# Kernel optimization log

Measured on AMD Instinct MI355X. Metric: run time of the kernel, lower is better.

The kernel has to match this reference:

```python
import jax, jax.numpy as jnp
import numpy as np

B, S, D_MODEL = 2, 2048, 1024
N_HEADS, N_KV_HEADS, D_HEAD = 16, 4, 64
N_GROUPS = N_HEADS // N_KV_HEADS
ATTN_SCALE = 1.0 / np.sqrt(D_HEAD)  # qk_scale_factor=1.0
LOGIT_SOFTCAP = 15.0
WINDOW = 256
N_GLOBAL = 4
EPS = 1e-8


def _l2_normalize(x):
    norm = jnp.linalg.norm(x, axis=-1, keepdims=True)
    return x / (norm + EPS)


def _apply_rope(t, cos, sin):
    # t: (B, H, S, D); cos/sin: (S, D//2)
    half = t.shape[-1] // 2
    x1, x2 = t[..., :half], t[..., half:]
    c = cos[None, None, :, :]
    s = sin[None, None, :, :]
    return jnp.concatenate([x1 * c - x2 * s, x1 * s + x2 * c], axis=-1)


def _sliding_window_mask(seq_len, window, n_global):
    q = jnp.arange(seq_len)[:, None]
    k = jnp.arange(seq_len)[None, :]
    causal = k <= q
    in_window = k > q - window
    is_global = k < n_global
    return (causal & in_window | is_global)[None, None, :, :]


def setup_inputs() -> dict:
    key = jax.random.key(0)
    ks = jax.random.split(key, 7)
    x = jax.random.normal(ks[0], (B, S, D_MODEL), dtype=jnp.float32)
    # RoPE tables from standard inverse-frequency construction
    inv_freq = 1.0 / (10000.0 ** (jnp.arange(0, D_HEAD, 2, dtype=jnp.float32) / D_HEAD))
    angles = jnp.arange(S, dtype=jnp.float32)[:, None] * inv_freq[None, :]  # (S, D_HEAD//2)
    cos = jnp.cos(angles)
    sin = jnp.sin(angles)
    # causal mask supplied by caller (TransformerLM): (1,1,S,S) bool, True = attend
    mask = (jnp.arange(S)[None, :] <= jnp.arange(S)[:, None])[None, None, :, :]
    scale_in = 1.0 / np.sqrt(D_MODEL)
    Wq = jax.random.normal(ks[1], (D_MODEL, N_HEADS * D_HEAD), dtype=jnp.float32) * scale_in
    Wk = jax.random.normal(ks[2], (D_MODEL, N_KV_HEADS * D_HEAD), dtype=jnp.float32) * scale_in
    Wv = jax.random.normal(ks[3], (D_MODEL, N_KV_HEADS * D_HEAD), dtype=jnp.float32) * scale_in
    Wo = jax.random.normal(ks[4], (N_HEADS * D_HEAD, D_MODEL), dtype=jnp.float32) * (1.0 / np.sqrt(N_HEADS * D_HEAD))
    return {"x": x, "cos": cos, "sin": sin, "mask": mask, "Wq": Wq, "Wk": Wk, "Wv": Wv, "Wo": Wo}


def reference(x, cos, sin, mask, Wq, Wk, Wv, Wo):
    Bb, Ss, _ = x.shape
    q = (x @ Wq).reshape(Bb, Ss, N_HEADS, D_HEAD).transpose(0, 2, 1, 3)      # (B,H,S,D)
    k = (x @ Wk).reshape(Bb, Ss, N_KV_HEADS, D_HEAD).transpose(0, 2, 1, 3)   # (B,Hkv,S,D)
    v = (x @ Wv).reshape(Bb, Ss, N_KV_HEADS, D_HEAD).transpose(0, 2, 1, 3)
    # QK L2 normalization (in fp32)
    q = _l2_normalize(q.astype(jnp.float32)).astype(q.dtype)
    k = _l2_normalize(k.astype(jnp.float32)).astype(k.dtype)
    # RoPE
    q = _apply_rope(q, cos, sin)
    k = _apply_rope(k, cos, sin)
    # GQA: expand kv heads
    k_exp = jnp.repeat(k, N_GROUPS, axis=1)
    v_exp = jnp.repeat(v, N_GROUPS, axis=1)
    scores = jnp.einsum('bhqd,bhkd->bhqk', q.astype(jnp.float32), k_exp.astype(jnp.float32)) * ATTN_SCALE
    scores = LOGIT_SOFTCAP * jnp.tanh(scores / LOGIT_SOFTCAP)
    window_mask = _sliding_window_mask(Ss, WINDOW, N_GLOBAL)
    combined = mask & window_mask
    scores = jnp.where(combined, scores, jnp.float32(-1e9))
    weights = jax.nn.softmax(scores, axis=-1)
    context = jnp.einsum('bhqk,bhkd->bhqd', weights, v_exp.astype(jnp.float32))
    context = context.transpose(0, 2, 1, 3).reshape(Bb, Ss, N_HEADS * D_HEAD).astype(x.dtype)
    return context @ Wo
```

## Files before the change

### kernel.cpp

```cpp
#include <hip/hip_runtime.h>
#include <hip/hip_bf16.h>

#define BATCH 2
#define SLEN 2048
#define DMODEL 1024
#define NHEADS 16
#define NKV 4
#define DHEAD 64
#define WINDOW 256
#define NGLOBAL 4

typedef __attribute__((ext_vector_type(8))) short short8;
typedef __attribute__((ext_vector_type(4))) float floatx4;

__device__ __forceinline__ ushort f2bf(float f) {
    __hip_bfloat16 h = __float2bfloat16(f);
    return *reinterpret_cast<ushort*>(&h);
}
__device__ __forceinline__ float bf2f(ushort u) {
    __hip_bfloat16 h = *reinterpret_cast<__hip_bfloat16*>(&u);
    return __bfloat162float(h);
}
__device__ __forceinline__ bool is_bf16_inputs(const uint* cosu) {
    return (cosu[0] & 0xFFFFu) != 0u;
}
__device__ __forceinline__ void gload_lds16(const ushort* g, ushort* l) {
    __builtin_amdgcn_global_load_lds(
        (const __attribute__((address_space(1))) void*)g,
        (__attribute__((address_space(3))) void*)l, 16, 0, 0);
}

__global__ __launch_bounds__(256) void prep_all(const void* __restrict__ x,
                                                const void* __restrict__ cosi,
                                                const void* __restrict__ sini,
                                                const void* __restrict__ Wq,
                                                const void* __restrict__ Wk,
                                                const void* __restrict__ Wv,
                                                const void* __restrict__ Wo,
                                                ushort* __restrict__ xb,
                                                float* __restrict__ cosf,
                                                float* __restrict__ sinf,
                                                ushort* __restrict__ Wt,
                                                ushort* __restrict__ Wot,
                                                const uint* __restrict__ cosu)
{
    __shared__ ushort t[32][33];
    const bool isbf = is_bf16_inputs(cosu);
    const int bid = blockIdx.x, tid = threadIdx.x;
    if (bid < 2048) {
        size_t i = (size_t)bid * 256 + tid;
        size_t e = i * 8;
        if (isbf) {
            *reinterpret_cast<uint4*>(xb + e) = reinterpret_cast<const uint4*>(x)[i];
        } else {
            const float* f = reinterpret_cast<const float*>(x) + e;
            ushort o[8];
#pragma unroll
            for (int j = 0; j < 8; ++j) o[j] = f2bf(f[j]);
            *reinterpret_cast<uint4*>(xb + e) = *reinterpret_cast<uint4*>(o);
        }
        return;
    }
    if (bid < 2560) {
        int i = (bid - 2048) * 256 + tid;
        const void* src = (i < SLEN * 32) ? cosi : sini;
        float* dst = (i < SLEN * 32) ? cosf : sinf;
        int e = i & (SLEN * 32 - 1);
        dst[e] = isbf ? bf2f(reinterpret_cast<const ushort*>(src)[e])
                      : reinterpret_cast<const float*>(src)[e];
        return;
    }
    const void* src; ushort* dst; int C, tl;
    if (bid < 3584)      { src = Wq; dst = Wt;                       C = 1024; tl = bid - 2560; }
    else if (bid < 3840) { src = Wk; dst = Wt + (size_t)1024 * 1024; C = 256;  tl = bid - 3584; }
    else if (bid < 4096) { src = Wv; dst = Wt + (size_t)1280 * 1024; C = 256;  tl = bid - 3840; }
    else                 { src = Wo; dst = Wot;                      C = 1024; tl = bid - 4096; }
    const int nbx = C >> 5;
    const int bx = (tl % nbx) * 32, by = (tl / nbx) * 32;
    const int tx = tid & 31, ty = tid >> 5;
#pragma unroll
    for (int j = 0; j < 32; j += 8) {
        size_t idx = (size_t)(by + ty + j) * C + bx + tx;
        t[ty + j][tx] = isbf ? reinterpret_cast<const ushort*>(src)[idx]
                             : f2bf(reinterpret_cast<const float*>(src)[idx]);
    }
    __syncthreads();
#pragma unroll
    for (int j = 0; j < 32; j += 8)
        dst[(size_t)(bx + ty + j) * 1024 + by + tx] = t[tx][ty + j];
}

__global__ __launch_bounds__(256) void gemm_qkv_nr(const ushort* __restrict__ A,
                                                   const ushort* __restrict__ Bt,
                                                   const float* __restrict__ cosf,
                                                   const float* __restrict__ sinf,
                                                   ushort* __restrict__ Qb,
                                                   ushort* __restrict__ Kg,
                                                   ushort* __restrict__ Vtg)
{
    __shared__ __align__(16) ushort buf[12288];
    ushort* lsA = buf;
    ushort* lsB = buf + 8192;
    const int tid = threadIdx.x;
    const int lane = tid & 63, w = tid >> 6;
    const int ln15 = lane & 15, quad = lane >> 4;
    const int z = blockIdx.x;
    const int rm = blockIdx.y * 128;
    const int cn = z * 64;

    floatx4 acc[2][4];
#pragma unroll
    for (int i = 0; i < 2; ++i)
#pragma unroll
        for (int j = 0; j < 4; ++j) acc[i][j] = (floatx4){0.f, 0.f, 0.f, 0.f};

    for (int k0 = 0; k0 < 1024; k0 += 64) {
        __syncthreads();
#pragma unroll
        for (int i = 0; i < 4; ++i) {
            const int c = (i * 4 + w) * 64 + lane;
            const int row = c >> 3, col = (c & 7) * 8;
            gload_lds16(&A[(size_t)(rm + row) * 1024 + k0 + col], &lsA[(i * 4 + w) * 512]);
        }
#pragma unroll
        for (int i = 0; i < 2; ++i) {
            const int c = (w * 2 + i) * 64 + lane;
            const int row = c >> 3, col = (c & 7) * 8;
            gload_lds16(&Bt[(size_t)(cn + row) * 1024 + k0 + col], &lsB[(w * 2 + i) * 512]);
        }
        __syncthreads();
#pragma unroll
        for (int kk = 0; kk < 64; kk += 32) {
            short8 af[2], bv[4];
#pragma unroll
            for (int i = 0; i < 2; ++i)
                af[i] = *reinterpret_cast<const short8*>(&lsA[(w * 32 + i * 16 + ln15) * 64 + kk + quad * 8]);
#pragma unroll
            for (int j = 0; j < 4; ++j)
                bv[j] = *reinterpret_cast<const short8*>(&lsB[(j * 16 + ln15) * 64 + kk + quad * 8]);
#pragma unroll
            for (int i = 0; i < 2; ++i)
#pragma unroll
                for (int j = 0; j < 4; ++j)
                    acc[i][j] = __builtin_amdgcn_mfma_f32_16x16x32_bf16(af[i], bv[j], acc[i][j], 0, 0, 0);
        }
    }

    __syncthreads();
    const int b = rm >> 11, s0 = rm & (SLEN - 1);

    if (z < 20) {
#pragma unroll
        for (int i = 0; i < 2; ++i) {
#pragma unroll
            for (int r = 0; r < 4; ++r) {
                const int row_l = w * 32 + i * 16 + quad * 4 + r;
                float v0 = acc[i][0][r], v1 = acc[i][1][r], v2 = acc[i][2][r], v3 = acc[i][3][r];
                float ss = v0 * v0 + v1 * v1 + v2 * v2 + v3 * v3;
                ss += __shfl_xor(ss, 1, 64);
                ss += __shfl_xor(ss, 2, 64);
                ss += __shfl_xor(ss, 4, 64);
                ss += __shfl_xor(ss, 8, 64);
                const float inv = 1.f / (sqrtf(ss) + 1e-8f);
                const float n0 = v0 * inv, n1 = v1 * inv, n2 = v2 * inv, n3 = v3 * inv;
                const int spos = s0 + row_l;
                const float c0 = cosf[spos * 32 + ln15],      c1 = cosf[spos * 32 + 16 + ln15];
                const float sn0 = sinf[spos * 32 + ln15],     sn1 = sinf[spos * 32 + 16 + ln15];
                buf[row_l * 72 + ln15]      = f2bf(n0 * c0 - n2 * sn0);
                buf[row_l * 72 + 16 + ln15] = f2bf(n1 * c1 - n3 * sn1);
                buf[row_l * 72 + 32 + ln15] = f2bf(n0 * sn0 + n2 * c0);
                buf[row_l * 72 + 48 + ln15] = f2bf(n1 * sn1 + n3 * c1);
            }
        }
        __syncthreads();
        ushort* dst = (z < 16) ? Qb + ((size_t)(b * NHEADS + z) * SLEN + s0) * 64
                               : Kg + ((size_t)(b * NKV + (z - 16)) * SLEN + s0) * 64;
#pragma unroll
        for (int it = 0; it < 4; ++it) {
            const int c = it * 256 + tid;
            const int row = c >> 3, col = (c & 7) * 8;
            *reinterpret_cast<uint4*>(dst + (size_t)row * 64 + col) =
                *reinterpret_cast<const uint4*>(&buf[row * 72 + col]);
        }
    } else {
#pragma unroll
        for (int i = 0; i < 2; ++i)
#pragma unroll
            for (int r = 0; r < 4; ++r) {
                const int row_l = w * 32 + i * 16 + quad * 4 + r;
#pragma unroll
                for (int j = 0; j < 4; ++j)
                    buf[(j * 16 + ln15) * 136 + row_l] = f2bf(acc[i][j][r]);
            }
        __syncthreads();
        ushort* dst = Vtg + ((size_t)(b * NKV + (z - 20)) * 64) * SLEN;
#pragma unroll
        for (int it = 0; it < 4; ++it) {
            const int c = it * 256 + tid;
            const int d = c >> 4, sb = (c & 15) * 8;
            *reinterpret_cast<uint4*>(dst + (size_t)d * SLEN + s0 + sb) =
                *reinterpret_cast<const uint4*>(&buf[d * 136 + sb]);
        }
    }
}

__global__ __launch_bounds__(256) void attn_mfma(const ushort* __restrict__ Qb,
                                                 const ushort* __restrict__ Kg,
                                                 const ushort* __restrict__ Vtg,
                                                 ushort* __restrict__ ctx)
{
    __shared__ ushort Ks[64 * 72];
    __shared__ ushort Vs[64 * 72];
    __shared__ ushort Ps[4][16 * 72];

    const int tid = threadIdx.x;
    const int lane = tid & 63, w = tid >> 6;
    const int ln15 = lane & 15, quad = lane >> 4;
    const int bid = blockIdx.x;
    const int qt = bid & 31, bh = bid >> 5;
    const int h = bh & (NHEADS - 1), b = bh >> 4, hkv = h >> 2;
    const int q0 = qt * 64;
    const int qw = q0 + w * 16;

    const ushort* Qrow = Qb + ((size_t)bh * SLEN + qw) * 64;
    const ushort* Kbase = Kg + (size_t)(b * NKV + hkv) * SLEN * 64;
    const ushort* Vbase = Vtg + (size_t)(b * NKV + hkv) * 64 * SLEN;

    short8 qf0 = *reinterpret_cast<const short8*>(Qrow + (size_t)ln15 * 64 + quad * 8);
    short8 qf1 = *reinterpret_cast<const short8*>(Qrow + (size_t)ln15 * 64 + 32 + quad * 8);

    floatx4 O0 = {0,0,0,0}, O1 = {0,0,0,0}, O2 = {0,0,0,0}, O3 = {0,0,0,0};
    float lp[4] = {0.f, 0.f, 0.f, 0.f};

    int kminA = q0 - (WINDOW - 1); if (kminA < 0) kminA = 0;
    kminA &= ~63;
    const int gmax = kminA < NGLOBAL ? kminA : NGLOBAL;
    const int nc = (q0 + 64 - kminA) >> 6;

    for (int c = (gmax > 0 ? -1 : 0); c < nc; ++c) {
        const int kbase = (c < 0) ? 0 : kminA + c * 64;
        __syncthreads();
#pragma unroll
        for (int j = 0; j < 2; ++j) {
            const int c2 = tid + j * 256;
            const int row = c2 >> 3, col = (c2 & 7) * 8;
            *reinterpret_cast<uint4*>(&Ks[row * 72 + col]) =
                *reinterpret_cast<const uint4*>(&Kbase[(size_t)(kbase + row) * 64 + col]);
            *reinterpret_cast<uint4*>(&Vs[row * 72 + col]) =
                *reinterpret_cast<const uint4*>(&Vbase[(size_t)row * SLEN + kbase + col]);
        }
        __syncthreads();

#pragma unroll
        for (int t = 0; t < 4; ++t) {
            short8 kf0 = *reinterpret_cast<const short8*>(&Ks[(t * 16 + ln15) * 72 + quad * 8]);
            short8 kf1 = *reinterpret_cast<const short8*>(&Ks[(t * 16 + ln15) * 72 + 32 + quad * 8]);
            floatx4 sc = {0,0,0,0};
            sc = __builtin_amdgcn_mfma_f32_16x16x32_bf16(qf0, kf0, sc, 0, 0, 0);
            sc = __builtin_amdgcn_mfma_f32_16x16x32_bf16(qf1, kf1, sc, 0, 0, 0);
            const int k = kbase + t * 16 + ln15;
#pragma unroll
            for (int r = 0; r < 4; ++r) {
                const int q = qw + quad * 4 + r;
                const bool valid = (c < 0) ? (k < gmax)
                                           : (k <= q && (k + WINDOW > q || k < NGLOBAL));
                float sv = sc[r] * 0.125f;
                float e2 = __expf(sv * 0.13333333f);
                float st = 15.f - 30.f * __builtin_amdgcn_rcpf(e2 + 1.f);
                ushort eb = valid ? f2bf(__expf(st)) : (ushort)0;
                Ps[w][(quad * 4 + r) * 72 + t * 16 + ln15] = eb;
                lp[r] += bf2f(eb);
            }
        }
        short8 af0 = *reinterpret_cast<const short8*>(&Ps[w][ln15 * 72 + quad * 8]);
        short8 af1 = *reinterpret_cast<const short8*>(&Ps[w][ln15 * 72 + 32 + quad * 8]);
#pragma unroll
        for (int n = 0; n < 4; ++n) {
            short8 vf0 = *reinterpret_cast<const short8*>(&Vs[(n * 16 + ln15) * 72 + quad * 8]);
            short8 vf1 = *reinterpret_cast<const short8*>(&Vs[(n * 16 + ln15) * 72 + 32 + quad * 8]);
            floatx4 On = (n == 0) ? O0 : (n == 1) ? O1 : (n == 2) ? O2 : O3;
            On = __builtin_amdgcn_mfma_f32_16x16x32_bf16(af0, vf0, On, 0, 0, 0);
            On = __builtin_amdgcn_mfma_f32_16x16x32_bf16(af1, vf1, On, 0, 0, 0);
            if (n == 0) O0 = On; else if (n == 1) O1 = On; else if (n == 2) O2 = On; else O3 = On;
        }
    }

#pragma unroll
    for (int r = 0; r < 4; ++r) {
#pragma unroll
        for (int off = 1; off < 16; off <<= 1)
            lp[r] += __shfl_xor(lp[r], off, 64);
        const float inv = __builtin_amdgcn_rcpf(lp[r]);
        const int q = qw + quad * 4 + r;
        ushort* crow = ctx + ((size_t)(b * SLEN + q)) * DMODEL + h * 64 + ln15;
        crow[0]  = f2bf(O0[r] * inv);
        crow[16] = f2bf(O1[r] * inv);
        crow[32] = f2bf(O2[r] * inv);
        crow[48] = f2bf(O3[r] * inv);
    }
}

__global__ __launch_bounds__(256) void gemm_out(const ushort* __restrict__ A,
                                                const ushort* __restrict__ Bt,
                                                void* __restrict__ out,
                                                const uint* __restrict__ cosu)
{
    __shared__ __align__(16) ushort buf[12288];
    ushort* lsA = buf;
    ushort* lsB = buf + 8192;
    const int tid = threadIdx.x;
    const int lane = tid & 63, w = tid >> 6;
    const int ln15 = lane & 15, quad = lane >> 4;
    const int rm = blockIdx.y * 128;
    const int cn = blockIdx.x * 64;

    floatx4 acc[2][4];
#pragma unroll
    for (int i = 0; i < 2; ++i)
#pragma unroll
        for (int j = 0; j < 4; ++j) acc[i][j] = (floatx4){0.f, 0.f, 0.f, 0.f};

    for (int k0 = 0; k0 < 1024; k0 += 64) {
        __syncthreads();
#pragma unroll
        for (int i = 0; i < 4; ++i) {
            const int c = (i * 4 + w) * 64 + lane;
            const int row = c >> 3, col = (c & 7) * 8;
            gload_lds16(&A[(size_t)(rm + row) * 1024 + k0 + col], &lsA[(i * 4 + w) * 512]);
        }
#pragma unroll
        for (int i = 0; i < 2; ++i) {
            const int c = (w * 2 + i) * 64 + lane;
            const int row = c >> 3, col = (c & 7) * 8;
            gload_lds16(&Bt[(size_t)(cn + row) * 1024 + k0 + col], &lsB[(w * 2 + i) * 512]);
        }
        __syncthreads();
#pragma unroll
        for (int kk = 0; kk < 64; kk += 32) {
            short8 af[2], bv[4];
#pragma unroll
            for (int i = 0; i < 2; ++i)
                af[i] = *reinterpret_cast<const short8*>(&lsA[(w * 32 + i * 16 + ln15) * 64 + kk + quad * 8]);
#pragma unroll
            for (int j = 0; j < 4; ++j)
                bv[j] = *reinterpret_cast<const short8*>(&lsB[(j * 16 + ln15) * 64 + kk + quad * 8]);
#pragma unroll
            for (int i = 0; i < 2; ++i)
#pragma unroll
                for (int j = 0; j < 4; ++j)
                    acc[i][j] = __builtin_amdgcn_mfma_f32_16x16x32_bf16(af[i], bv[j], acc[i][j], 0, 0, 0);
        }
    }

    const bool outbf = is_bf16_inputs(cosu);
#pragma unroll
    for (int i = 0; i < 2; ++i) {
#pragma unroll
        for (int r = 0; r < 4; ++r) {
            const int grow = rm + w * 32 + i * 16 + quad * 4 + r;
#pragma unroll
            for (int j = 0; j < 4; ++j) {
                const int gcol = cn + j * 16 + ln15;
                if (outbf) reinterpret_cast<ushort*>(out)[(size_t)grow * DMODEL + gcol] = f2bf(acc[i][j][r]);
                else       reinterpret_cast<float*>(out)[(size_t)grow * DMODEL + gcol] = acc[i][j][r];
            }
        }
    }
}

extern "C" void kernel_launch(void* const* d_in, const int* in_sizes, int n_in,
                              void* d_out, int out_size, void* d_ws, size_t ws_size,
                              hipStream_t stream)
{
    (void)in_sizes; (void)n_in; (void)out_size; (void)ws_size;
    const void* x = d_in[0];
    const void* cosi = d_in[1];
    const void* sini = d_in[2];
    const uint* cosu = (const uint*)d_in[1];
    const void* Wq = d_in[4];
    const void* Wk = d_in[5];
    const void* Wv = d_in[6];
    const void* Wo = d_in[7];

    ushort* xb = (ushort*)d_ws;
    ushort* Wt = xb + (size_t)4096 * 1024;
    ushort* Wot = Wt + (size_t)1536 * 1024;
    float* cosf = (float*)(Wot + (size_t)1024 * 1024);
    float* sinf = cosf + (size_t)SLEN * 32;
    ushort* Qbf = (ushort*)(sinf + (size_t)SLEN * 32);
    ushort* Kgf = Qbf + (size_t)BATCH * NHEADS * SLEN * 64;
    ushort* Vtg = Kgf + (size_t)BATCH * NKV * SLEN * 64;
    ushort* ctx = Vtg + (size_t)BATCH * NKV * 64 * SLEN;

    prep_all<<<dim3(5120), 256, 0, stream>>>(x, cosi, sini, Wq, Wk, Wv, Wo,
                                             xb, cosf, sinf, Wt, Wot, cosu);

    gemm_qkv_nr<<<dim3(24, 32), 256, 0, stream>>>(xb, Wt, cosf, sinf, Qbf, Kgf, Vtg);

    attn_mfma<<<dim3(BATCH * NHEADS * SLEN / 64), 256, 0, stream>>>(Qbf, Kgf, Vtg, ctx);

    gemm_out<<<dim3(16, 32), 256, 0, stream>>>(ctx, Wot, d_out, cosu);
}
```

Measured before the change: 166.1 us.

## Fuse prep, QKV GEMM, attention and output GEMM into one cooperative persistent kernel

Replaces the four separate kernel launches with a single cooperative megakernel that loops over virtual blocks per stage and separates stages with grid-wide syncs. This is meant to remove launch gaps and tail effects between stages. The output GEMM is retiled to 64x64 tiles to give more tiles. Softcap tanh is replaced by a cubic Taylor approximation, and row sums now use unrounded fp32 probabilities. The change risks grid.sync overhead, lower occupancy under the fused register budget, and accuracy loss from the tanh approximation.

```diff
diff --git a/kernel.cpp b/kernel.cpp
--- a/kernel.cpp
+++ b/kernel.cpp
@@ -1,5 +1,8 @@
 #include <hip/hip_runtime.h>
 #include <hip/hip_bf16.h>
+#include <hip/hip_cooperative_groups.h>
+
+namespace cg = cooperative_groups;
 
 #define BATCH 2
 #define SLEN 2048
@@ -30,340 +33,305 @@
         (__attribute__((address_space(3))) void*)l, 16, 0, 0);
 }
 
-__global__ __launch_bounds__(256) void prep_all(const void* __restrict__ x,
-                                                const void* __restrict__ cosi,
-                                                const void* __restrict__ sini,
-                                                const void* __restrict__ Wq,
-                                                const void* __restrict__ Wk,
-                                                const void* __restrict__ Wv,
-                                                const void* __restrict__ Wo,
-                                                ushort* __restrict__ xb,
-                                                float* __restrict__ cosf,
-                                                float* __restrict__ sinf,
-                                                ushort* __restrict__ Wt,
-                                                ushort* __restrict__ Wot,
-                                                const uint* __restrict__ cosu)
+__global__ __launch_bounds__(256, 4) void mega(
+    const void* __restrict__ x, const void* __restrict__ cosi, const void* __restrict__ sini,
+    const void* __restrict__ Wq, const void* __restrict__ Wk,
+    const void* __restrict__ Wv, const void* __restrict__ Wo,
+    ushort* __restrict__ xb, float* __restrict__ cosf_, float* __restrict__ sinf_,
+    ushort* __restrict__ Wt, ushort* __restrict__ Wot,
+    ushort* __restrict__ Qb, ushort* __restrict__ Kg, ushort* __restrict__ Vtg,
+    ushort* __restrict__ ctx, void* __restrict__ out,
+    const uint* __restrict__ cosu, int nblk)
 {
-    __shared__ ushort t[32][33];
-    const bool isbf = is_bf16_inputs(cosu);
-    const int bid = blockIdx.x, tid = threadIdx.x;
-    if (bid < 2048) {
-        size_t i = (size_t)bid * 256 + tid;
-        size_t e = i * 8;
-        if (isbf) {
-            *reinterpret_cast<uint4*>(xb + e) = reinterpret_cast<const uint4*>(x)[i];
-        } else {
-            const float* f = reinterpret_cast<const float*>(x) + e;
-            ushort o[8];
-#pragma unroll
-            for (int j = 0; j < 8; ++j) o[j] = f2bf(f[j]);
-            *reinterpret_cast<uint4*>(xb + e) = *reinterpret_cast<uint4*>(o);
-        }
-        return;
-    }
-    if (bid < 2560) {
-        int i = (bid - 2048) * 256 + tid;
-        const void* src = (i < SLEN * 32) ? cosi : sini;
-        float* dst = (i < SLEN * 32) ? cosf : sinf;
-        int e = i & (SLEN * 32 - 1);
-        dst[e] = isbf ? bf2f(reinterpret_cast<const ushort*>(src)[e])
-                      : reinterpret_cast<const float*>(src)[e];
-        return;
-    }
-    const void* src; ushort* dst; int C, tl;
-    if (bid < 3584)      { src = Wq; dst = Wt;                       C = 1024; tl = bid - 2560; }
-    else if (bid < 3840) { src = Wk; dst = Wt + (size_t)1024 * 1024; C = 256;  tl = bid - 3584; }
-    else if (bid < 4096) { src = Wv; dst = Wt + (size_t)1280 * 1024; C = 256;  tl = bid - 3840; }
-    else                 { src = Wo; dst = Wot;                      C = 1024; tl = bid - 4096; }
-    const int nbx = C >> 5;
-    const int bx = (tl % nbx) * 32, by = (tl / nbx) * 32;
-    const int tx = tid & 31, ty = tid >> 5;
-#pragma unroll
-    for (int j = 0; j < 32; j += 8) {
-        size_t idx = (size_t)(by + ty + j) * C + bx + tx;
-        t[ty + j][tx] = isbf ? reinterpret_cast<const ushort*>(src)[idx]
-                             : f2bf(reinterpret_cast<const float*>(src)[idx]);
-    }
-    __syncthreads();
-#pragma unroll
-    for (int j = 0; j < 32; j += 8)
-        dst[(size_t)(bx + ty + j) * 1024 + by + tx] = t[tx][ty + j];
-}
-
-__global__ __launch_bounds__(256) void gemm_qkv_nr(const ushort* __restrict__ A,
-                                                   const ushort* __restrict__ Bt,
-                                                   const float* __restrict__ cosf,
-                                                   const float* __restrict__ sinf,
-                                                   ushort* __restrict__ Qb,
-                                                   ushort* __restrict__ Kg,
-                                                   ushort* __restrict__ Vtg)
-{
-    __shared__ __align__(16) ushort buf[12288];
-    ushort* lsA = buf;
-    ushort* lsB = buf + 8192;
+    __shared__ __align__(16) ushort sm[13824];
+    cg::grid_group grid = cg::this_grid();
     const int tid = threadIdx.x;
+    const int blk = blockIdx.x;
     const int lane = tid & 63, w = tid >> 6;
     const int ln15 = lane & 15, quad = lane >> 4;
-    const int z = blockIdx.x;
-    const int rm = blockIdx.y * 128;
-    const int cn = z * 64;
-
-    floatx4 acc[2][4];
-#pragma unroll
-    for (int i = 0; i < 2; ++i)
-#pragma unroll
-        for (int j = 0; j < 4; ++j) acc[i][j] = (floatx4){0.f, 0.f, 0.f, 0.f};
-
-    for (int k0 = 0; k0 < 1024; k0 += 64) {
-        __syncthreads();
-#pragma unroll
-        for (int i = 0; i < 4; ++i) {
-            const int c = (i * 4 + w) * 64 + lane;
-            const int row = c >> 3, col = (c & 7) * 8;
-            gload_lds16(&A[(size_t)(rm + row) * 1024 + k0 + col], &lsA[(i * 4 + w) * 512]);
-        }
-#pragma unroll
-        for (int i = 0; i < 2; ++i) {
-            const int c = (w * 2 + i) * 64 + lane;
-            const int row = c >> 3, col = (c & 7) * 8;
-            gload_lds16(&Bt[(size_t)(cn + row) * 1024 + k0 + col], &lsB[(w * 2 + i) * 512]);
+    const bool isbf = is_bf16_inputs(cosu);
+
+    for (int vb = blk; vb < 5120; vb += nblk) {
+        if (vb < 2048) {
+            size_t i = (size_t)vb * 256 + tid;
+            size_t e = i * 8;
+            if (isbf) {
+                *reinterpret_cast<uint4*>(xb + e) = reinterpret_cast<const uint4*>(x)[i];
+            } else {
+                const float* f = reinterpret_cast<const float*>(x) + e;
+                ushort o[8];
+#pragma unroll
+                for (int j = 0; j < 8; ++j) o[j] = f2bf(f[j]);
+                *reinterpret_cast<uint4*>(xb + e) = *reinterpret_cast<uint4*>(o);
+            }
+        } else if (vb < 2560) {
+            int i = (vb - 2048) * 256 + tid;
+            const void* src = (i < SLEN * 32) ? cosi : sini;
+            float* dst = (i < SLEN * 32) ? cosf_ : sinf_;
+            int e = i & (SLEN * 32 - 1);
+            dst[e] = isbf ? bf2f(reinterpret_cast<const ushort*>(src)[e])
+                          : reinterpret_cast<const float*>(src)[e];
+        } else {
+            const void* src; ushort* dst; int C, tl;
+            if (vb < 3584)      { src = Wq; dst = Wt;                       C = 1024; tl = vb - 2560; }
+            else if (vb < 3840) { src = Wk; dst = Wt + (size_t)1024 * 1024; C = 256;  tl = vb - 3584; }
+            else if (vb < 4096) { src = Wv; dst = Wt + (size_t)1280 * 1024; C = 256;  tl = vb - 3840; }
+            else                { src = Wo; dst = Wot;                      C = 1024; tl = vb - 4096; }
+            const int nbx = C >> 5;
+            const int bx = (tl % nbx) * 32, by = (tl / nbx) * 32;
+            const int tx = tid & 31, ty = tid >> 5;
+            ushort (*t)[33] = reinterpret_cast<ushort(*)[33]>(sm);
+#pragma unroll
+            for (int j = 0; j < 32; j += 8) {
+                size_t idx = (size_t)(by + ty + j) * C + bx + tx;
+                t[ty + j][tx] = isbf ? reinterpret_cast<const ushort*>(src)[idx]
+                                     : f2bf(reinterpret_cast<const float*>(src)[idx]);
+            }
+            __syncthreads();
+#pragma unroll
+            for (int j = 0; j < 32; j += 8)
+                dst[(size_t)(bx + ty + j) * 1024 + by + tx] = t[tx][ty + j];
         }
         __syncthreads();
-#pragma unroll
-        for (int kk = 0; kk < 64; kk += 32) {
-            short8 af[2], bv[4];
+    }
+    grid.sync();
+
+    {
+        ushort* lsA = sm;
+        ushort* lsB = sm + 8192;
+        for (int tile = blk; tile < 768; tile += nblk) {
+            const int z = tile % 24;
+            const int rm = (tile / 24) * 128;
+            const int cn = z * 64;
+
+            floatx4 acc[2][4];
 #pragma unroll
             for (int i = 0; i < 2; ++i)
-                af[i] = *reinterpret_cast<const short8*>(&lsA[(w * 32 + i * 16 + ln15) * 64 + kk + quad * 8]);
-#pragma unroll
-            for (int j = 0; j < 4; ++j)
-                bv[j] = *reinterpret_cast<const short8*>(&lsB[(j * 16 + ln15) * 64 + kk + quad * 8]);
-#pragma unroll
-            for (int i = 0; i < 2; ++i)
-#pragma unroll
-                for (int j = 0; j < 4; ++j)
-                    acc[i][j] = __builtin_amdgcn_mfma_f32_16x16x32_bf16(af[i], bv[j], acc[i][j], 0, 0, 0);
+#pragma unroll
+                for (int j = 0; j < 4; ++j) acc[i][j] = (floatx4){0.f, 0.f, 0.f, 0.f};
+
+            for (int k0 = 0; k0 < 1024; k0 += 64) {
+                __syncthreads();
+#pragma unroll
+                for (int i = 0; i < 4; ++i) {
+                    const int c = (i * 4 + w) * 64 + lane;
+                    const int row = c >> 3, col = (c & 7) * 8;
+                    gload_lds16(&xb[(size_t)(rm + row) * 1024 + k0 + col], &lsA[(i * 4 + w) * 512]);
+                }
+#pragma unroll
+                for (int i = 0; i < 2; ++i) {
+                    const int c = (w * 2 + i) * 64 + lane;
+                    const int row = c >> 3, col = (c & 7) * 8;
+                    gload_lds16(&Wt[(size_t)(cn + row) * 1024 + k0 + col], &lsB[(w * 2 + i) * 512]);
+                }
+                __syncthreads();
+#pragma unroll
+                for (int kk = 0; kk < 64; kk += 32) {
+                    short8 af[2], bv[4];
+#pragma unroll
+                    for (int i = 0; i < 2; ++i)
+                        af[i] = *reinterpret_cast<const short8*>(&lsA[(w * 32 + i * 16 + ln15) * 64 + kk + quad * 8]);
+#pragma unroll
+                    for (int j = 0; j < 4; ++j)
+                        bv[j] = *reinterpret_cast<const short8*>(&lsB[(j * 16 + ln15) * 64 + kk + quad * 8]);
+#pragma unroll
+                    for (int i = 0; i < 2; ++i)
+#pragma unroll
+                        for (int j = 0; j < 4; ++j)
+                            acc[i][j] = __builtin_amdgcn_mfma_f32_16x16x32_bf16(af[i], bv[j], acc[i][j], 0, 0, 0);
+                }
+            }
+
+            __syncthreads();
+            const int b = rm >> 11, s0 = rm & (SLEN - 1);
+            if (z < 20) {
+#pragma unroll
+                for (int i = 0; i < 2; ++i) {
+#pragma unroll
+                    for (int r = 0; r < 4; ++r) {
+                        const int row_l = w * 32 + i * 16 + quad * 4 + r;
+                        float v0 = acc[i][0][r], v1 = acc[i][1][r], v2 = acc[i][2][r], v3 = acc[i][3][r];
+                        float ss = v0 * v0 + v1 * v1 + v2 * v2 + v3 * v3;
+                        ss += __shfl_xor(ss, 1, 64);
+                        ss += __shfl_xor(ss, 2, 64);
+                        ss += __shfl_xor(ss, 4, 64);
+                        ss += __shfl_xor(ss, 8, 64);
+                        const float inv = 1.f / (sqrtf(ss) + 1e-8f);
+                        const float n0 = v0 * inv, n1 = v1 * inv, n2 = v2 * inv, n3 = v3 * inv;
+                        const int spos = s0 + row_l;
+                        const float c0 = cosf_[spos * 32 + ln15],  c1 = cosf_[spos * 32 + 16 + ln15];
+                        const float sn0 = sinf_[spos * 32 + ln15], sn1 = sinf_[spos * 32 + 16 + ln15];
+                        sm[row_l * 72 + ln15]      = f2bf(n0 * c0 - n2 * sn0);
+                        sm[row_l * 72 + 16 + ln15] = f2bf(n1 * c1 - n3 * sn1);
+                        sm[row_l * 72 + 32 + ln15] = f2bf(n0 * sn0 + n2 * c0);
+                        sm[row_l * 72 + 48 + ln15] = f2bf(n1 * sn1 + n3 * c1);
+                    }
+                }
+                __syncthreads();
+                ushort* dst = (z < 16) ? Qb + ((size_t)(b * NHEADS + z) * SLEN + s0) * 64
+                                       : Kg + ((size_t)(b * NKV + (z - 16)) * SLEN + s0) * 64;
+#pragma unroll
+                for (int it = 0; it < 4; ++it) {
+                    const int c = it * 256 + tid;
+                    const int row = c >> 3, col = (c & 7) * 8;
+                    *reinterpret_cast<uint4*>(dst + (size_t)row * 64 + col) =
+                        *reinterpret_cast<const uint4*>(&sm[row * 72 + col]);
+                }
+            } else {
+#pragma unroll
+                for (int i = 0; i < 2; ++i)
+#pragma unroll
+                    for (int r = 0; r < 4; ++r) {
+                        const int row_l = w * 32 + i * 16 + quad * 4 + r;
+#pragma unroll
+                        for (int j = 0; j < 4; ++j)
+                            sm[(j * 16 + ln15) * 136 + row_l] = f2bf(acc[i][j][r]);
+                    }
+                __syncthreads();
+                ushort* dst = Vtg + ((size_t)(b * NKV + (z - 20)) * 64) * SLEN;
+#pragma unroll
+                for (int it = 0; it < 4; ++it) {
+                    const int c = it * 256 + tid;
+                    const int d = c >> 4, sb = (c & 15) * 8;
+                    *reinterpret_cast<uint4*>(dst + (size_t)d * SLEN + s0 + sb) =
+                        *reinterpret_cast<const uint4*>(&sm[d * 136 + sb]);
+                }
+            }
+            __syncthreads();
         }
     }
-
-    __syncthreads();
-    const int b = rm >> 11, s0 = rm & (SLEN - 1);
-
-    if (z < 20) {
-#pragma unroll
-        for (int i = 0; i < 2; ++i) {
+    grid.sync();
+
+    {
+        ushort* Ks = sm;
+        ushort* Vs = sm + 4608;
+        ushort* Ps = sm + 9216 + w * 1152;
+        for (int tile = blk; tile < 1024; tile += nblk) {
+            const int qt = tile & 31, bh = tile >> 5;
+            const int h = bh & (NHEADS - 1), b = bh >> 4, hkv = h >> 2;
+            const int q0 = qt * 64;
+            const int qw = q0 + w * 16;
+
+            const ushort* Qrow = Qb + ((size_t)bh * SLEN + qw) * 64;
+            const ushort* Kbase = Kg + (size_t)(b * NKV + hkv) * SLEN * 64;
+            const ushort* Vbase = Vtg + (size_t)(b * NKV + hkv) * 64 * SLEN;
+
+            short8 qf0 = *reinterpret_cast<const short8*>(Qrow + (size_t)ln15 * 64 + quad * 8);
+            short8 qf1 = *reinterpret_cast<const short8*>(Qrow + (size_t)ln15 * 64 + 32 + quad * 8);
+
+            floatx4 O0 = {0,0,0,0}, O1 = {0,0,0,0}, O2 = {0,0,0,0}, O3 = {0,0,0,0};
+            float lp[4] = {0.f, 0.f, 0.f, 0.f};
+
+            int kminA = q0 - (WINDOW - 1); if (kminA < 0) kminA = 0;
+            kminA &= ~63;
+            const int gmax = kminA < NGLOBAL ? kminA : NGLOBAL;
+            const int nc = (q0 + 64 - kminA) >> 6;
+
+            for (int c = (gmax > 0 ? -1 : 0); c < nc; ++c) {
+                const int kbase = (c < 0) ? 0 : kminA + c * 64;
+                __syncthreads();
+#pragma unroll
+                for (int j = 0; j < 2; ++j) {
+                    const int c2 = tid + j * 256;
+                    const int row = c2 >> 3, col = (c2 & 7) * 8;
+                    *reinterpret_cast<uint4*>(&Ks[row * 72 + col]) =
+                        *reinterpret_cast<const uint4*>(&Kbase[(size_t)(kbase + row) * 64 + col]);
+                    *reinterpret_cast<uint4*>(&Vs[row * 72 + col]) =
+                        *reinterpret_cast<const uint4*>(&Vbase[(size_t)row * SLEN + kbase + col]);
+                }
+                __syncthreads();
+
+#pragma unroll
+                for (int t = 0; t < 4; ++t) {
+                    short8 kf0 = *reinterpret_cast<const short8*>(&Ks[(t * 16 + ln15) * 72 + quad * 8]);
+                    short8 kf1 = *reinterpret_cast<const short8*>(&Ks[(t * 16 + ln15) * 72 + 32 + quad * 8]);
+                    floatx4 sc = {0,0,0,0};
+                    sc = __builtin_amdgcn_mfma_f32_16x16x32_bf16(qf0, kf0, sc, 0, 0, 0);
+                    sc = __builtin_amdgcn_mfma_f32_16x16x32_bf16(qf1, kf1, sc, 0, 0, 0);
+                    const int k = kbase + t * 16 + ln15;
+#pragma unroll
+                    for (int r = 0; r < 4; ++r) {
+                        const int q = qw + quad * 4 + r;
+                        const bool valid = (c < 0) ? (k < gmax)
+                                                   : (k <= q && (k + WINDOW > q || k < NGLOBAL));
+                        float sv = sc[r] * 0.125f;
+                        float st = sv - sv * sv * sv * (1.0f / 675.0f);
+                        float p = __expf(st);
+                        Ps[(quad * 4 + r) * 72 + t * 16 + ln15] = valid ? f2bf(p) : (ushort)0;
+                        lp[r] += valid ? p : 0.f;
+                    }
+                }
+                short8 af0 = *reinterpret_cast<const short8*>(&Ps[ln15 * 72 + quad * 8]);
+                short8 af1 = *reinterpret_cast<const short8*>(&Ps[ln15 * 72 + 32 + quad * 8]);
+#pragma unroll
+                for (int n = 0; n < 4; ++n) {
+                    short8 vf0 = *reinterpret_cast<const short8*>(&Vs[(n * 16 + ln15) * 72 + quad * 8]);
+                    short8 vf1 = *reinterpret_cast<const short8*>(&Vs[(n * 16 + ln15) * 72 + 32 + quad * 8]);
+                    floatx4 On = (n == 0) ? O0 : (n == 1) ? O1 : (n == 2) ? O2 : O3;
+                    On = __builtin_amdgcn_mfma_f32_16x16x32_bf16(af0, vf0, On, 0, 0, 0);
+                    On = __builtin_amdgcn_mfma_f32_16x16x32_bf16(af1, vf1, On, 0, 0, 0);
+                    if (n == 0) O0 = On; else if (n == 1) O1 = On; else if (n == 2) O2 = On; else O3 = On;
+                }
+            }
+
 #pragma unroll
             for (int r = 0; r < 4; ++r) {
-                const int row_l = w * 32 + i * 16 + quad * 4 + r;
-                float v0 = acc[i][0][r], v1 = acc[i][1][r], v2 = acc[i][2][r], v3 = acc[i][3][r];
-                float ss = v0 * v0 + v1 * v1 + v2 * v2 + v3 * v3;
-                ss += __shfl_xor(ss, 1, 64);
-                ss += __shfl_xor(ss, 2, 64);
-                ss += __shfl_xor(ss, 4, 64);
-                ss += __shfl_xor(ss, 8, 64);
-                const float inv = 1.f / (sqrtf(ss) + 1e-8f);
-                const float n0 = v0 * inv, n1 = v1 * inv, n2 = v2 * inv, n3 = v3 * inv;
-                const int spos = s0 + row_l;
-                const float c0 = cosf[spos * 32 + ln15],      c1 = cosf[spos * 32 + 16 + ln15];
-                const float sn0 = sinf[spos * 32 + ln15],     sn1 = sinf[spos * 32 + 16 + ln15];
-                buf[row_l * 72 + ln15]      = f2bf(n0 * c0 - n2 * sn0);
-                buf[row_l * 72 + 16 + ln15] = f2bf(n1 * c1 - n3 * sn1);
-                buf[row_l * 72 + 32 + ln15] = f2bf(n0 * sn0 + n2 * c0);
-                buf[row_l * 72 + 48 + ln15] = f2bf(n1 * sn1 + n3 * c1);
-            }
-        }
-        __syncthreads();
-        ushort* dst = (z < 16) ? Qb + ((size_t)(b * NHEADS + z) * SLEN + s0) * 64
-                               : Kg + ((size_t)(b * NKV + (z - 16)) * SLEN + s0) * 64;
-#pragma unroll
-        for (int it = 0; it < 4; ++it) {
-            const int c = it * 256 + tid;
-            const int row = c >> 3, col = (c & 7) * 8;
-            *reinterpret_cast<uint4*>(dst + (size_t)row * 64 + col) =
-                *reinterpret_cast<const uint4*>(&buf[row * 72 + col]);
-        }
-    } else {
-#pragma unroll
-        for (int i = 0; i < 2; ++i)
-#pragma unroll
-            for (int r = 0; r < 4; ++r) {
-                const int row_l = w * 32 + i * 16 + quad * 4 + r;
-#pragma unroll
-                for (int j = 0; j < 4; ++j)
-                    buf[(j * 16 + ln15) * 136 + row_l] = f2bf(acc[i][j][r]);
-            }
-        __syncthreads();
-        ushort* dst = Vtg + ((size_t)(b * NKV + (z - 20)) * 64) * SLEN;
-#pragma unroll
-        for (int it = 0; it < 4; ++it) {
-            const int c = it * 256 + tid;
-            const int d = c >> 4, sb = (c & 15) * 8;
-            *reinterpret_cast<uint4*>(dst + (size_t)d * SLEN + s0 + sb) =
-                *reinterpret_cast<const uint4*>(&buf[d * 136 + sb]);
+#pragma unroll
+                for (int off = 1; off < 16; off <<= 1)
+                    lp[r] += __shfl_xor(lp[r], off, 64);
+                const float inv = __builtin_amdgcn_rcpf(lp[r]);
+                const int q = qw + quad * 4 + r;
+                ushort* crow = ctx + ((size_t)(b * SLEN + q)) * DMODEL + h * 64 + ln15;
+                crow[0]  = f2bf(O0[r] * inv);
+                crow[16] = f2bf(O1[r] * inv);
+                crow[32] = f2bf(O2[r] * inv);
+                crow[48] = f2bf(O3[r] * inv);
+            }
+            __syncthreads();
         }
     }
-}
-
-__global__ __launch_bounds__(256) void attn_mfma(const ushort* __restrict__ Qb,
-                                                 const ushort* __restrict__ Kg,
-                                                 const ushort* __restrict__ Vtg,
-                                                 ushort* __restrict__ ctx)
-{
-    __shared__ ushort Ks[64 * 72];
-    __shared__ ushort Vs[64 * 72];
-    __shared__ ushort Ps[4][16 * 72];
-
-    const int tid = threadIdx.x;
-    const int lane = tid & 63, w = tid >> 6;
-    const int ln15 = lane & 15, quad = lane >> 4;
-    const int bid = blockIdx.x;
-    const int qt = bid & 31, bh = bid >> 5;
-    const int h = bh & (NHEADS - 1), b = bh >> 4, hkv = h >> 2;
-    const int q0 = qt * 64;
-    const int qw = q0 + w * 16;
-
-    const ushort* Qrow = Qb + ((size_t)bh * SLEN + qw) * 64;
-    const ushort* Kbase = Kg + (size_t)(b * NKV + hkv) * SLEN * 64;
-    const ushort* Vbase = Vtg + (size_t)(b * NKV + hkv) * 64 * SLEN;
-
-    short8 qf0 = *reinterpret_cast<const short8*>(Qrow + (size_t)ln15 * 64 + quad * 8);
-    short8 qf1 = *reinterpret_cast<const short8*>(Qrow + (size_t)ln15 * 64 + 32 + quad * 8);
-
-    floatx4 O0 = {0,0,0,0}, O1 = {0,0,0,0}, O2 = {0,0,0,0}, O3 = {0,0,0,0};
-    float lp[4] = {0.f, 0.f, 0.f, 0.f};
-
-    int kminA = q0 - (WINDOW - 1); if (kminA < 0) kminA = 0;
-    kminA &= ~63;
-    const int gmax = kminA < NGLOBAL ? kminA : NGLOBAL;
-    const int nc = (q0 + 64 - kminA) >> 6;
-
-    for (int c = (gmax > 0 ? -1 : 0); c < nc; ++c) {
-        const int kbase = (c < 0) ? 0 : kminA + c * 64;
-        __syncthreads();
-#pragma unroll
-        for (int j = 0; j < 2; ++j) {
-            const int c2 = tid + j * 256;
-            const int row = c2 >> 3, col = (c2 & 7) * 8;
-            *reinterpret_cast<uint4*>(&Ks[row * 72 + col]) =
-                *reinterpret_cast<const uint4*>(&Kbase[(size_t)(kbase + row) * 64 + col]);
-            *reinterpret_cast<uint4*>(&Vs[row * 72 + col]) =
-                *reinterpret_cast<const uint4*>(&Vbase[(size_t)row * SLEN + kbase + col]);
-        }
-        __syncthreads();
-
-#pragma unroll
-        for (int t = 0; t < 4; ++t) {
-            short8 kf0 = *reinterpret_cast<const short8*>(&Ks[(t * 16 + ln15) * 72 + quad * 8]);
-            short8 kf1 = *reinterpret_cast<const short8*>(&Ks[(t * 16 + ln15) * 72 + 32 + quad * 8]);
-            floatx4 sc = {0,0,0,0};
-            sc = __builtin_amdgcn_mfma_f32_16x16x32_bf16(qf0, kf0, sc, 0, 0, 0);
-            sc = __builtin_amdgcn_mfma_f32_16x16x32_bf16(qf1, kf1, sc, 0, 0, 0);
-            const int k = kbase + t * 16 + ln15;
+    grid.sync();
+
+    {
+        ushort* lsA = sm;
+        ushort* lsB = sm + 4096;
+        for (int tile = blk; tile < 1024; tile += nblk) {
+            const int rm = (tile >> 4) * 64, cn = (tile & 15) * 64;
+            floatx4 acc[4];
+#pragma unroll
+            for (int j = 0; j < 4; ++j) acc[j] = (floatx4){0.f, 0.f, 0.f, 0.f};
+
+            for (int k0 = 0; k0 < 1024; k0 += 64) {
+                __syncthreads();
+#pragma unroll
+                for (int i = 0; i < 2; ++i) {
+                    const int c = (w * 2 + i) * 64 + lane;
+                    const int row = c >> 3, col = (c & 7) * 8;
+                    gload_lds16(&ctx[(size_t)(rm + row) * 1024 + k0 + col], &lsA[(w * 2 + i) * 512]);
+                    gload_lds16(&Wot[(size_t)(cn + row) * 1024 + k0 + col], &lsB[(w * 2 + i) * 512]);
+                }
+                __syncthreads();
+#pragma unroll
+                for (int kk = 0; kk < 64; kk += 32) {
+                    short8 af = *reinterpret_cast<const short8*>(&lsA[(w * 16 + ln15) * 64 + kk + quad * 8]);
+#pragma unroll
+                    for (int j = 0; j < 4; ++j) {
+                        short8 bv = *reinterpret_cast<const short8*>(&lsB[(j * 16 + ln15) * 64 + kk + quad * 8]);
+                        acc[j] = __builtin_amdgcn_mfma_f32_16x16x32_bf16(af, bv, acc[j], 0, 0, 0);
+                    }
+                }
+            }
 #pragma unroll
             for (int r = 0; r < 4; ++r) {
-                const int q = qw + quad * 4 + r;
-                const bool valid = (c < 0) ? (k < gmax)
-                                           : (k <= q && (k + WINDOW > q || k < NGLOBAL));
-                float sv = sc[r] * 0.125f;
-                float e2 = __expf(sv * 0.13333333f);
-                float st = 15.f - 30.f * __builtin_amdgcn_rcpf(e2 + 1.f);
-                ushort eb = valid ? f2bf(__expf(st)) : (ushort)0;
-                Ps[w][(quad * 4 + r) * 72 + t * 16 + ln15] = eb;
-                lp[r] += bf2f(eb);
-            }
-        }
-        short8 af0 = *reinterpret_cast<const short8*>(&Ps[w][ln15 * 72 + quad * 8]);
-        short8 af1 = *reinterpret_cast<const short8*>(&Ps[w][ln15 * 72 + 32 + quad * 8]);
-#pragma unroll
-        for (int n = 0; n < 4; ++n) {
-            short8 vf0 = *reinterpret_cast<const short8*>(&Vs[(n * 16 + ln15) * 72 + quad * 8]);
-            short8 vf1 = *reinterpret_cast<const short8*>(&Vs[(n * 16 + ln15) * 72 + 32 + quad * 8]);
-            floatx4 On = (n == 0) ? O0 : (n == 1) ? O1 : (n == 2) ? O2 : O3;
-            On = __builtin_amdgcn_mfma_f32_16x16x32_bf16(af0, vf0, On, 0, 0, 0);
-            On = __builtin_amdgcn_mfma_f32_16x16x32_bf16(af1, vf1, On, 0, 0, 0);
-            if (n == 0) O0 = On; else if (n == 1) O1 = On; else if (n == 2) O2 = On; else O3 = On;
-        }
-    }
-
-#pragma unroll
-    for (int r = 0; r < 4; ++r) {
-#pragma unroll
-        for (int off = 1; off < 16; off <<= 1)
-            lp[r] += __shfl_xor(lp[r], off, 64);
-        const float inv = __builtin_amdgcn_rcpf(lp[r]);
-        const int q = qw + quad * 4 + r;
-        ushort* crow = ctx + ((size_t)(b * SLEN + q)) * DMODEL + h * 64 + ln15;
-        crow[0]  = f2bf(O0[r] * inv);
-        crow[16] = f2bf(O1[r] * inv);
-        crow[32] = f2bf(O2[r] * inv);
-        crow[48] = f2bf(O3[r] * inv);
-    }
-}
-
-__global__ __launch_bounds__(256) void gemm_out(const ushort* __restrict__ A,
-                                                const ushort* __restrict__ Bt,
-                                                void* __restrict__ out,
-                                                const uint* __restrict__ cosu)
-{
-    __shared__ __align__(16) ushort buf[12288];
-    ushort* lsA = buf;
-    ushort* lsB = buf + 8192;
-    const int tid = threadIdx.x;
-    const int lane = tid & 63, w = tid >> 6;
-    const int ln15 = lane & 15, quad = lane >> 4;
-    const int rm = blockIdx.y * 128;
-    const int cn = blockIdx.x * 64;
-
-    floatx4 acc[2][4];
-#pragma unroll
-    for (int i = 0; i < 2; ++i)
-#pragma unroll
-        for (int j = 0; j < 4; ++j) acc[i][j] = (floatx4){0.f, 0.f, 0.f, 0.f};
-
-    for (int k0 = 0; k0 < 1024; k0 += 64) {
-        __syncthreads();
-#pragma unroll
-        for (int i = 0; i < 4; ++i) {
-            const int c = (i * 4 + w) * 64 + lane;
-            const int row = c >> 3, col = (c & 7) * 8;
-            gload_lds16(&A[(size_t)(rm + row) * 1024 + k0 + col], &lsA[(i * 4 + w) * 512]);
-        }
-#pragma unroll
-        for (int i = 0; i < 2; ++i) {
-            const int c = (w * 2 + i) * 64 + lane;
-            const int row = c >> 3, col = (c & 7) * 8;
-            gload_lds16(&Bt[(size_t)(cn + row) * 1024 + k0 + col], &lsB[(w * 2 + i) * 512]);
-        }
-        __syncthreads();
-#pragma unroll
-        for (int kk = 0; kk < 64; kk += 32) {
-            short8 af[2], bv[4];
-#pragma unroll
-            for (int i = 0; i < 2; ++i)
-                af[i] = *reinterpret_cast<const short8*>(&lsA[(w * 32 + i * 16 + ln15) * 64 + kk + quad * 8]);
-#pragma unroll
-            for (int j = 0; j < 4; ++j)
-                bv[j] = *reinterpret_cast<const short8*>(&lsB[(j * 16 + ln15) * 64 + kk + quad * 8]);
-#pragma unroll
-            for (int i = 0; i < 2; ++i)
-#pragma unroll
-                for (int j = 0; j < 4; ++j)
-                    acc[i][j] = __builtin_amdgcn_mfma_f32_16x16x32_bf16(af[i], bv[j], acc[i][j], 0, 0, 0);
-        }
-    }
-
-    const bool outbf = is_bf16_inputs(cosu);
-#pragma unroll
-    for (int i = 0; i < 2; ++i) {
-#pragma unroll
-        for (int r = 0; r < 4; ++r) {
-            const int grow = rm + w * 32 + i * 16 + quad * 4 + r;
-#pragma unroll
-            for (int j = 0; j < 4; ++j) {
-                const int gcol = cn + j * 16 + ln15;
-                if (outbf) reinterpret_cast<ushort*>(out)[(size_t)grow * DMODEL + gcol] = f2bf(acc[i][j][r]);
-                else       reinterpret_cast<float*>(out)[(size_t)grow * DMODEL + gcol] = acc[i][j][r];
-            }
+                const int grow = rm + w * 16 + quad * 4 + r;
+#pragma unroll
+                for (int j = 0; j < 4; ++j) {
+                    const int gcol = cn + j * 16 + ln15;
+                    if (isbf) reinterpret_cast<ushort*>(out)[(size_t)grow * DMODEL + gcol] = f2bf(acc[j][r]);
+                    else      reinterpret_cast<float*>(out)[(size_t)grow * DMODEL + gcol] = acc[j][r];
+                }
+            }
+            __syncthreads();
         }
     }
 }
@@ -385,19 +353,24 @@
     ushort* xb = (ushort*)d_ws;
     ushort* Wt = xb + (size_t)4096 * 1024;
     ushort* Wot = Wt + (size_t)1536 * 1024;
-    float* cosf = (float*)(Wot + (size_t)1024 * 1024);
-    float* sinf = cosf + (size_t)SLEN * 32;
-    ushort* Qbf = (ushort*)(sinf + (size_t)SLEN * 32);
+    float* cosf_ = (float*)(Wot + (size_t)1024 * 1024);
+    float* sinf_ = cosf_ + (size_t)SLEN * 32;
+    ushort* Qbf = (ushort*)(sinf_ + (size_t)SLEN * 32);
     ushort* Kgf = Qbf + (size_t)BATCH * NHEADS * SLEN * 64;
     ushort* Vtg = Kgf + (size_t)BATCH * NKV * SLEN * 64;
     ushort* ctx = Vtg + (size_t)BATCH * NKV * 64 * SLEN;
 
-    prep_all<<<dim3(5120), 256, 0, stream>>>(x, cosi, sini, Wq, Wk, Wv, Wo,
-                                             xb, cosf, sinf, Wt, Wot, cosu);
-
-    gemm_qkv_nr<<<dim3(24, 32), 256, 0, stream>>>(xb, Wt, cosf, sinf, Qbf, Kgf, Vtg);
-
-    attn_mfma<<<dim3(BATCH * NHEADS * SLEN / 64), 256, 0, stream>>>(Qbf, Kgf, Vtg, ctx);
-
-    gemm_out<<<dim3(16, 32), 256, 0, stream>>>(ctx, Wot, d_out, cosu);
-}
+    int perCU = 0;
+    hipOccupancyMaxActiveBlocksPerMultiprocessor(&perCU, (const void*)mega, 256, 0);
+    if (perCU < 1) perCU = 1;
+    int nblk = perCU * 256;
+    if (nblk > 1024) nblk = 1024;
+
+    void* kx = (void*)x; void* kc = (void*)cosi; void* ks = (void*)sini;
+    void* kq = (void*)Wq; void* kk = (void*)Wk; void* kv = (void*)Wv; void* ko = (void*)Wo;
+    void* kcu = (void*)cosu; void* kout = d_out;
+    void* args[] = { &kx, &kc, &ks, &kq, &kk, &kv, &ko,
+                     &xb, &cosf_, &sinf_, &Wt, &Wot,
+                     &Qbf, &Kgf, &Vtg, &ctx, &kout, &kcu, &nblk };
+    hipLaunchCooperativeKernel((const void*)mega, dim3(nblk), dim3(256), args, 0, stream);
+}
```

After: 391.9 us. 136% more time.

## Pad GEMM LDS tiles to 72-element rows and approximate softcap tanh with cubic

Applied to the files above, without the earlier changes.

Both GEMM kernels now stage A and B tiles into LDS with a 72-element padded row stride, using extra dummy 16-byte direct-to-LDS loads to fill the padding, to cut LDS bank conflicts on the MFMA fragment reads. Separately, the attention kernel replaces the exp/rcp tanh softcap with a cubic Taylor approximation (s - s^3/675) and accumulates the row sum in fp32 rather than from bf16-rounded values. The cubic only matches tanh for small scores, which holds here because q and k are L2-normalized. It removes transcendental work per score at some accuracy cost.

```diff
diff --git a/kernel.cpp b/kernel.cpp
--- a/kernel.cpp
+++ b/kernel.cpp
@@ -28,6 +28,15 @@
     __builtin_amdgcn_global_load_lds(
         (const __attribute__((address_space(1))) void*)g,
         (__attribute__((address_space(3))) void*)l, 16, 0, 0);
+}
+
+__device__ __forceinline__ void stage_row(const ushort* gbase, size_t gstride, int k0,
+                                          ushort* lds, int call, int lane) {
+    const int c2 = call * 64 + lane;
+    const int srow = c2 / 9;
+    const int rem = c2 - srow * 9;
+    const int colu = (rem == 8) ? 0 : rem * 8;
+    gload_lds16(&gbase[(size_t)srow * gstride + k0 + colu], &lds[call * 512]);
 }
 
 __global__ __launch_bounds__(256) void prep_all(const void* __restrict__ x,
@@ -98,9 +107,9 @@
                                                    ushort* __restrict__ Kg,
                                                    ushort* __restrict__ Vtg)
 {
-    __shared__ __align__(16) ushort buf[12288];
-    ushort* lsA = buf;
-    ushort* lsB = buf + 8192;
+    __shared__ __align__(16) ushort sm[13824];
+    ushort* lsA = sm;
+    ushort* lsB = sm + 9216;
     const int tid = threadIdx.x;
     const int lane = tid & 63, w = tid >> 6;
     const int ln15 = lane & 15, quad = lane >> 4;
@@ -114,19 +123,20 @@
 #pragma unroll
         for (int j = 0; j < 4; ++j) acc[i][j] = (floatx4){0.f, 0.f, 0.f, 0.f};
 
+    const ushort* Ab = A + (size_t)rm * 1024;
+    const ushort* Bb = Bt + (size_t)cn * 1024;
+
     for (int k0 = 0; k0 < 1024; k0 += 64) {
         __syncthreads();
 #pragma unroll
-        for (int i = 0; i < 4; ++i) {
-            const int c = (i * 4 + w) * 64 + lane;
-            const int row = c >> 3, col = (c & 7) * 8;
-            gload_lds16(&A[(size_t)(rm + row) * 1024 + k0 + col], &lsA[(i * 4 + w) * 512]);
-        }
-#pragma unroll
-        for (int i = 0; i < 2; ++i) {
-            const int c = (w * 2 + i) * 64 + lane;
-            const int row = c >> 3, col = (c & 7) * 8;
-            gload_lds16(&Bt[(size_t)(cn + row) * 1024 + k0 + col], &lsB[(w * 2 + i) * 512]);
+        for (int i = 0; i < 5; ++i) {
+            const int call = i * 4 + w;
+            if (call < 18) stage_row(Ab, 1024, k0, lsA, call, lane);
+        }
+#pragma unroll
+        for (int i = 0; i < 3; ++i) {
+            const int call = i * 4 + w;
+            if (call < 9) stage_row(Bb, 1024, k0, lsB, call, lane);
         }
         __syncthreads();
 #pragma unroll
@@ -134,10 +144,10 @@
             short8 af[2], bv[4];
 #pragma unroll
             for (int i = 0; i < 2; ++i)
-                af[i] = *reinterpret_cast<const short8*>(&lsA[(w * 32 + i * 16 + ln15) * 64 + kk + quad * 8]);
+                af[i] = *reinterpret_cast<const short8*>(&lsA[(w * 32 + i * 16 + ln15) * 72 + kk + quad * 8]);
 #pragma unroll
             for (int j = 0; j < 4; ++j)
-                bv[j] = *reinterpret_cast<const short8*>(&lsB[(j * 16 + ln15) * 64 + kk + quad * 8]);
+                bv[j] = *reinterpret_cast<const short8*>(&lsB[(j * 16 + ln15) * 72 + kk + quad * 8]);
 #pragma unroll
             for (int i = 0; i < 2; ++i)
 #pragma unroll
@@ -148,7 +158,6 @@
 
     __syncthreads();
     const int b = rm >> 11, s0 = rm & (SLEN - 1);
-
     if (z < 20) {
 #pragma unroll
         for (int i = 0; i < 2; ++i) {
@@ -164,12 +173,12 @@
                 const float inv = 1.f / (sqrtf(ss) + 1e-8f);
                 const float n0 = v0 * inv, n1 = v1 * inv, n2 = v2 * inv, n3 = v3 * inv;
                 const int spos = s0 + row_l;
-                const float c0 = cosf[spos * 32 + ln15],      c1 = cosf[spos * 32 + 16 + ln15];
-                const float sn0 = sinf[spos * 32 + ln15],     sn1 = sinf[spos * 32 + 16 + ln15];
-                buf[row_l * 72 + ln15]      = f2bf(n0 * c0 - n2 * sn0);
-                buf[row_l * 72 + 16 + ln15] = f2bf(n1 * c1 - n3 * sn1);
-                buf[row_l * 72 + 32 + ln15] = f2bf(n0 * sn0 + n2 * c0);
-                buf[row_l * 72 + 48 + ln15] = f2bf(n1 * sn1 + n3 * c1);
+                const float c0 = cosf[spos * 32 + ln15],  c1 = cosf[spos * 32 + 16 + ln15];
+                const float sn0 = sinf[spos * 32 + ln15], sn1 = sinf[spos * 32 + 16 + ln15];
+                sm[row_l * 72 + ln15]      = f2bf(n0 * c0 - n2 * sn0);
+                sm[row_l * 72 + 16 + ln15] = f2bf(n1 * c1 - n3 * sn1);
+                sm[row_l * 72 + 32 + ln15] = f2bf(n0 * sn0 + n2 * c0);
+                sm[row_l * 72 + 48 + ln15] = f2bf(n1 * sn1 + n3 * c1);
             }
         }
         __syncthreads();
@@ -180,7 +189,7 @@
             const int c = it * 256 + tid;
             const int row = c >> 3, col = (c & 7) * 8;
             *reinterpret_cast<uint4*>(dst + (size_t)row * 64 + col) =
-                *reinterpret_cast<const uint4*>(&buf[row * 72 + col]);
+                *reinterpret_cast<const uint4*>(&sm[row * 72 + col]);
         }
     } else {
 #pragma unroll
@@ -190,7 +199,7 @@
                 const int row_l = w * 32 + i * 16 + quad * 4 + r;
 #pragma unroll
                 for (int j = 0; j < 4; ++j)
-                    buf[(j * 16 + ln15) * 136 + row_l] = f2bf(acc[i][j][r]);
+                    sm[(j * 16 + ln15) * 136 + row_l] = f2bf(acc[i][j][r]);
             }
         __syncthreads();
         ushort* dst = Vtg + ((size_t)(b * NKV + (z - 20)) * 64) * SLEN;
@@ -199,7 +208,7 @@
             const int c = it * 256 + tid;
             const int d = c >> 4, sb = (c & 15) * 8;
             *reinterpret_cast<uint4*>(dst + (size_t)d * SLEN + s0 + sb) =
-                *reinterpret_cast<const uint4*>(&buf[d * 136 + sb]);
+                *reinterpret_cast<const uint4*>(&sm[d * 136 + sb]);
         }
     }
 }
@@ -265,11 +274,10 @@
                 const bool valid = (c < 0) ? (k < gmax)
                                            : (k <= q && (k + WINDOW > q || k < NGLOBAL));
                 float sv = sc[r] * 0.125f;
-                float e2 = __expf(sv * 0.13333333f);
-                float st = 15.f - 30.f * __builtin_amdgcn_rcpf(e2 + 1.f);
-                ushort eb = valid ? f2bf(__expf(st)) : (ushort)0;
-                Ps[w][(quad * 4 + r) * 72 + t * 16 + ln15] = eb;
-                lp[r] += bf2f(eb);
+                float st = sv - sv * sv * sv * (1.0f / 675.0f);
+                float p = __expf(st);
+                Ps[w][(quad * 4 + r) * 72 + t * 16 + ln15] = valid ? f2bf(p) : (ushort)0;
+                lp[r] += valid ? p : 0.f;
             }
         }
         short8 af0 = *reinterpret_cast<const short8*>(&Ps[w][ln15 * 72 + quad * 8]);
@@ -305,9 +313,9 @@
                                                 void* __restrict__ out,
                                                 const uint* __restrict__ cosu)
 {
-    __shared__ __align__(16) ushort buf[12288];
-    ushort* lsA = buf;
-    ushort* lsB = buf + 8192;
+    __shared__ __align__(16) ushort sm[13824];
+    ushort* lsA = sm;
+    ushort* lsB = sm + 9216;
     const int tid = threadIdx.x;
     const int lane = tid & 63, w = tid >> 6;
     const int ln15 = lane & 15, quad = lane >> 4;
@@ -320,19 +328,20 @@
 #pragma unroll
         for (int j = 0; j < 4; ++j) acc[i][j] = (floatx4){0.f, 0.f, 0.f, 0.f};
 
+    const ushort* Ab = A + (size_t)rm * 1024;
+    const ushort* Bb = Bt + (size_t)cn * 1024;
+
     for (int k0 = 0; k0 < 1024; k0 += 64) {
         __syncthreads();
 #pragma unroll
-        for (int i = 0; i < 4; ++i) {
-            const int c = (i * 4 + w) * 64 + lane;
-            const int row = c >> 3, col = (c & 7) * 8;
-            gload_lds16(&A[(size_t)(rm + row) * 1024 + k0 + col], &lsA[(i * 4 + w) * 512]);
-        }
-#pragma unroll
-        for (int i = 0; i < 2; ++i) {
-            const int c = (w * 2 + i) * 64 + lane;
-            const int row = c >> 3, col = (c & 7) * 8;
-            gload_lds16(&Bt[(size_t)(cn + row) * 1024 + k0 + col], &lsB[(w * 2 + i) * 512]);
+        for (int i = 0; i < 5; ++i) {
+            const int call = i * 4 + w;
+            if (call < 18) stage_row(Ab, 1024, k0, lsA, call, lane);
+        }
+#pragma unroll
+        for (int i = 0; i < 3; ++i) {
+            const int call = i * 4 + w;
+            if (call < 9) stage_row(Bb, 1024, k0, lsB, call, lane);
         }
         __syncthreads();
 #pragma unroll
@@ -340,10 +349,10 @@
             short8 af[2], bv[4];
 #pragma unroll
             for (int i = 0; i < 2; ++i)
-                af[i] = *reinterpret_cast<const short8*>(&lsA[(w * 32 + i * 16 + ln15) * 64 + kk + quad * 8]);
+                af[i] = *reinterpret_cast<const short8*>(&lsA[(w * 32 + i * 16 + ln15) * 72 + kk + quad * 8]);
 #pragma unroll
             for (int j = 0; j < 4; ++j)
-                bv[j] = *reinterpret_cast<const short8*>(&lsB[(j * 16 + ln15) * 64 + kk + quad * 8]);
+                bv[j] = *reinterpret_cast<const short8*>(&lsB[(j * 16 + ln15) * 72 + kk + quad * 8]);
 #pragma unroll
             for (int i = 0; i < 2; ++i)
 #pragma unroll
```

Result: faster. 155.1 us (-6.6%).
